# Performance work log

Measured on AMD Instinct MI355X. Metric: run time of the kernel, lower is better.

Reference implementation:

```python
import jax, jax.numpy as jnp
import numpy as np

HIDDEN = 128
NUM_VAL = 100000
NUM_CST = 20000
NUM_EDGES = 500000
LN_EPS = 1e-5


def layer_norm(x, g, b):
    mu = jnp.mean(x, axis=-1, keepdims=True)
    var = jnp.var(x, axis=-1, keepdims=True)
    return (x - mu) * jax.lax.rsqrt(var + LN_EPS) * g + b


def setup_inputs() -> dict:
    key = jax.random.key(0)
    ks = jax.random.split(key, 8)
    h_val = jax.random.normal(ks[0], (NUM_VAL, HIDDEN), dtype=jnp.float32)
    assign = jax.random.uniform(ks[1], (NUM_VAL,), dtype=jnp.float32)
    cst_src = jax.random.randint(ks[2], (NUM_EDGES,), 0, NUM_CST)  # constraint idx (scatter target)
    cst_dst = jax.random.randint(ks[3], (NUM_EDGES,), 0, NUM_VAL)  # value idx (gather source)
    LE = jax.random.randint(ks[4], (NUM_EDGES,), 0, 2)
    PE = jax.random.randint(ks[5], (NUM_EDGES,), 0, 2)
    s1 = 1.0 / np.sqrt(HIDDEN + 1)
    s2 = 1.0 / np.sqrt(HIDDEN)
    W1 = jax.random.normal(ks[6], (HIDDEN + 1, HIDDEN), dtype=jnp.float32) * s1
    b1 = jnp.zeros((HIDDEN,), dtype=jnp.float32)
    k7, k8 = jax.random.split(ks[7])
    W2 = jax.random.normal(k7, (HIDDEN, HIDDEN), dtype=jnp.float32) * s2
    W3 = jax.random.normal(k8, (HIDDEN, 4 * HIDDEN), dtype=jnp.float32) * s2
    return {
        "h_val": h_val, "assign": assign,
        "cst_src": cst_src, "cst_dst": cst_dst, "LE": LE, "PE": PE,
        "W1": W1, "b1": b1, "W2": W2,
        "ln1_g": jnp.ones((HIDDEN,), jnp.float32), "ln1_b": jnp.zeros((HIDDEN,), jnp.float32),
        "W3": W3,
        "ln2_g": jnp.ones((4 * HIDDEN,), jnp.float32), "ln2_b": jnp.zeros((4 * HIDDEN,), jnp.float32),
    }


def reference(h_val, assign, cst_src, cst_dst, LE, PE, W1, b1, W2, ln1_g, ln1_b, W3, ln2_g, ln2_b):
    # val_enc: Linear -> ReLU -> Linear(no bias) -> LayerNorm
    x = jnp.concatenate([h_val, assign[:, None]], axis=1)  # [V, H+1]
    x_val = layer_norm(jax.nn.relu(x @ W1 + b1) @ W2, ln1_g, ln1_b)  # [V, H]
    # val_send: Linear(no bias) -> LayerNorm over 4H, then view as [4V, H]
    m_val = layer_norm(x_val @ W3, ln2_g, ln2_b).reshape(4 * NUM_VAL, HIDDEN)
    # gather by composite edge index, scatter-sum into constraints
    out_idx = 4 * cst_dst + 2 * LE + PE  # [E]
    msg = m_val[out_idx]  # [E, H]
    r_cst = jax.ops.segment_sum(msg, cst_src, num_segments=NUM_CST)  # [C, H]
    return (r_cst, x_val)
```

## Files before the change

### kernel.cpp

```cpp
#include <hip/hip_runtime.h>
#include <hip/hip_bf16.h>

#define HID 128
#define NVAL 100000
#define NCST 20000
#define NEDGE 500000
#define LN_EPS 1e-5f
#define BCAP 96

#define ENC_BLOCKS  ((NVAL + 63) / 64)
#define SEND_BLOCKS (NVAL / 32)
#define WPACK_BLOCKS 48
#define SCT_BLOCKS  ((NEDGE + 255) / 256)

typedef __attribute__((ext_vector_type(8))) short bf16x8;
typedef __attribute__((ext_vector_type(4))) float f32x4;

static __device__ __forceinline__ unsigned short f2bf(float x) {
    union { float f; unsigned int u; } a; a.f = x;
    const unsigned int r = a.u + 0x7FFF + ((a.u >> 16) & 1);
    return (unsigned short)(r >> 16);
}
static __device__ __forceinline__ float bf2f(unsigned short u) {
    union { unsigned int i; float f; } x; x.i = (unsigned int)u << 16; return x.f;
}

__global__ __launch_bounds__(256) void k_phase1(
    const float* __restrict__ W1, const float* __restrict__ W2,
    const float* __restrict__ W3,
    unsigned short* __restrict__ PW1, unsigned short* __restrict__ PW2,
    unsigned short* __restrict__ PW3,
    const int* __restrict__ cst_src, const int* __restrict__ cst_dst,
    const int* __restrict__ LE, const int* __restrict__ PE,
    int* __restrict__ cnt, int* __restrict__ rows2)
{
    if (blockIdx.x < WPACK_BLOCKS) {
        const int g = blockIdx.x * 256 + threadIdx.x;
        const float* W; unsigned short* P; int gg, ncol;
        if (g < 2048)      { W = W1; P = PW1; gg = g;        ncol = 128; }
        else if (g < 4096) { W = W2; P = PW2; gg = g - 2048; ncol = 128; }
        else               { W = W3; P = PW3; gg = g - 4096; ncol = 512; }
        const int ct = gg >> 8, kc = (gg >> 6) & 3, l = gg & 63;
        const int col = ct * 16 + (l & 15);
        const int k0  = kc * 32 + (l >> 4) * 8;
        unsigned short tmp[8];
        #pragma unroll
        for (int j = 0; j < 8; ++j)
            tmp[j] = f2bf(W[(size_t)(k0 + j) * ncol + col]);
        *(bf16x8*)&P[(size_t)gg * 8] = *(const bf16x8*)tmp;
    } else {
        const int i = (blockIdx.x - WPACK_BLOCKS) * 256 + threadIdx.x;
        if (i < NEDGE) {
            const int s = cst_src[i];
            const int p = atomicAdd(&cnt[s], 1);
            if (p < BCAP)
                rows2[s * BCAP + p] = 4 * cst_dst[i] + 2 * LE[i] + PE[i];
        }
    }
}

__global__ __launch_bounds__(256) void k_val_enc_mfma(
    const float* __restrict__ h_val, const float* __restrict__ assign,
    const unsigned short* __restrict__ PW1, const float* __restrict__ W1,
    const float* __restrict__ b1, const unsigned short* __restrict__ PW2,
    const float* __restrict__ g1, const float* __restrict__ bb1,
    float* __restrict__ x_val, unsigned short* __restrict__ xb, int use_xb)
{
    __shared__ __align__(16) unsigned short AsHs[2 * 64 * 136];
    __shared__ float red[4][64][2];
    __shared__ float assn[64];

    unsigned short* As = AsHs;
    unsigned short* Hs = AsHs + 64 * 136;
    float* Os = (float*)AsHs;

    const int tid  = threadIdx.x;
    const int w    = tid >> 6;
    const int l    = tid & 63;
    const int row0 = blockIdx.x * 64;

    {
        const int r  = tid >> 2;
        const int c0 = (tid & 3) * 32;
        if (row0 + r < NVAL) {
            const float* src = h_val + (size_t)(row0 + r) * HID + c0;
            #pragma unroll
            for (int i = 0; i < 4; ++i) {
                const float4 va = *(const float4*)(src + i * 8);
                const float4 vb = *(const float4*)(src + i * 8 + 4);
                unsigned short h[8] = { f2bf(va.x), f2bf(va.y), f2bf(va.z), f2bf(va.w),
                                        f2bf(vb.x), f2bf(vb.y), f2bf(vb.z), f2bf(vb.w) };
                *(bf16x8*)&As[r * 136 + c0 + i * 8] = *(const bf16x8*)h;
            }
        } else {
            unsigned short z[8] = {0,0,0,0,0,0,0,0};
            #pragma unroll
            for (int i = 0; i < 4; ++i)
                *(bf16x8*)&As[r * 136 + c0 + i * 8] = *(const bf16x8*)z;
        }
    }
    if (tid < 64) assn[tid] = (row0 + tid < NVAL) ? assign[row0 + tid] : 0.0f;

    float b1c[2], wrc[2], g1c[2], bbc[2];
    #pragma unroll
    for (int ct = 0; ct < 2; ++ct) {
        const int col = (w * 2 + ct) * 16 + (l & 15);
        b1c[ct] = b1[col];
        wrc[ct] = W1[(size_t)128 * HID + col];
        g1c[ct] = g1[col];
        bbc[ct] = bb1[col];
    }

    __syncthreads();

    const int arow = l & 15;
    const int akb  = (l >> 4) * 8;

    f32x4 acc[4][2];
    #pragma unroll
    for (int rt = 0; rt < 4; ++rt)
        #pragma unroll
        for (int ct = 0; ct < 2; ++ct) acc[rt][ct] = (f32x4){0.f, 0.f, 0.f, 0.f};
    #pragma unroll
    for (int kc = 0; kc < 4; ++kc) {
        bf16x8 a[4];
        #pragma unroll
        for (int rt = 0; rt < 4; ++rt)
            a[rt] = *(const bf16x8*)&As[(arow + rt * 16) * 136 + kc * 32 + akb];
        #pragma unroll
        for (int ct = 0; ct < 2; ++ct) {
            const int ctg = w * 2 + ct;
            const bf16x8 b = *(const bf16x8*)&PW1[(size_t)((ctg * 4 + kc) * 64 + l) * 8];
            #pragma unroll
            for (int rt = 0; rt < 4; ++rt)
                acc[rt][ct] = __builtin_amdgcn_mfma_f32_16x16x32_bf16(a[rt], b, acc[rt][ct], 0, 0, 0);
        }
    }

    #pragma unroll
    for (int rt = 0; rt < 4; ++rt)
        #pragma unroll
        for (int ct = 0; ct < 2; ++ct) {
            const int col = (w * 2 + ct) * 16 + (l & 15);
            #pragma unroll
            for (int q = 0; q < 4; ++q) {
                const int row = rt * 16 + (l >> 4) * 4 + q;
                float v = acc[rt][ct][q] + b1c[ct] + assn[row] * wrc[ct];
                v = fmaxf(v, 0.0f);
                Hs[row * 136 + col] = f2bf(v);
            }
        }
    __syncthreads();

    f32x4 acc2[4][2];
    #pragma unroll
    for (int rt = 0; rt < 4; ++rt)
        #pragma unroll
        for (int ct = 0; ct < 2; ++ct) acc2[rt][ct] = (f32x4){0.f, 0.f, 0.f, 0.f};
    #pragma unroll
    for (int kc = 0; kc < 4; ++kc) {
        bf16x8 a[4];
        #pragma unroll
        for (int rt = 0; rt < 4; ++rt)
            a[rt] = *(const bf16x8*)&Hs[(arow + rt * 16) * 136 + kc * 32 + akb];
        #pragma unroll
        for (int ct = 0; ct < 2; ++ct) {
            const int ctg = w * 2 + ct;
            const bf16x8 b = *(const bf16x8*)&PW2[(size_t)((ctg * 4 + kc) * 64 + l) * 8];
            #pragma unroll
            for (int rt = 0; rt < 4; ++rt)
                acc2[rt][ct] = __builtin_amdgcn_mfma_f32_16x16x32_bf16(a[rt], b, acc2[rt][ct], 0, 0, 0);
        }
    }

    #pragma unroll
    for (int rt = 0; rt < 4; ++rt)
        #pragma unroll
        for (int q = 0; q < 4; ++q) {
            float s  = acc2[rt][0][q] + acc2[rt][1][q];
            float qq = acc2[rt][0][q] * acc2[rt][0][q] + acc2[rt][1][q] * acc2[rt][1][q];
            #pragma unroll
            for (int off2 = 1; off2 < 16; off2 <<= 1) {
                s  += __shfl_xor(s,  off2);
                qq += __shfl_xor(qq, off2);
            }
            if ((l & 15) == 0) {
                const int row = rt * 16 + (l >> 4) * 4 + q;
                red[w][row][0] = s;
                red[w][row][1] = qq;
            }
        }
    __syncthreads();

    #pragma unroll
    for (int rt = 0; rt < 4; ++rt)
        #pragma unroll
        for (int q = 0; q < 4; ++q) {
            const int row = rt * 16 + (l >> 4) * 4 + q;
            const float S = red[0][row][0] + red[1][row][0] + red[2][row][0] + red[3][row][0];
            const float Q = red[0][row][1] + red[1][row][1] + red[2][row][1] + red[3][row][1];
            const float mu  = S * (1.0f / 128.0f);
            const float var = Q * (1.0f / 128.0f) - mu * mu;
            const float rs  = rsqrtf(var + LN_EPS);
            #pragma unroll
            for (int ct = 0; ct < 2; ++ct) {
                const int col = (w * 2 + ct) * 16 + (l & 15);
                Os[row * 132 + col] = (acc2[rt][ct][q] - mu) * rs * g1c[ct] + bbc[ct];
            }
        }
    __syncthreads();

    {
        const int r  = tid >> 2;
        const int c0 = (tid & 3) * 32;
        if (row0 + r < NVAL) {
            float* dst = x_val + (size_t)(row0 + r) * HID + c0;
            #pragma unroll
            for (int i = 0; i < 8; ++i)
                *(float4*)(dst + i * 4) = *(const float4*)&Os[r * 132 + c0 + i * 4];
            if (use_xb) {
                unsigned short* db = xb + (size_t)(row0 + r) * HID + c0;
                #pragma unroll
                for (int i = 0; i < 4; ++i) {
                    const float4 va = *(const float4*)&Os[r * 132 + c0 + i * 8];
                    const float4 vb = *(const float4*)&Os[r * 132 + c0 + i * 8 + 4];
                    unsigned short h[8] = { f2bf(va.x), f2bf(va.y), f2bf(va.z), f2bf(va.w),
                                            f2bf(vb.x), f2bf(vb.y), f2bf(vb.z), f2bf(vb.w) };
                    *(bf16x8*)&db[i * 8] = *(const bf16x8*)h;
                }
            }
        }
    }
}

__global__ __launch_bounds__(256) void k_send(
    const float* __restrict__ x_val, const unsigned short* __restrict__ xb,
    const unsigned short* __restrict__ PB,
    const float* __restrict__ g2, const float* __restrict__ b2,
    unsigned short* __restrict__ m_val, int use_xb)
{
    __shared__ __align__(16) unsigned short U[16 * 520];
    __shared__ float red[4][32][2];

    unsigned short* As   = U;
    unsigned short* Os2h = U;

    const int tid  = threadIdx.x;
    const int w    = tid >> 6;
    const int l    = tid & 63;
    const int row0 = blockIdx.x * 32;

    if (use_xb) {
        const int r  = tid >> 3;
        const int c0 = (tid & 7) * 16;
        const unsigned short* src = xb + (size_t)(row0 + r) * HID + c0;
        *(bf16x8*)&As[r * 136 + c0]     = *(const bf16x8*)&src[0];
        *(bf16x8*)&As[r * 136 + c0 + 8] = *(const bf16x8*)&src[8];
    } else {
        const int r  = tid >> 3;
        const int c0 = (tid & 7) * 16;
        const float* src = x_val + (size_t)(row0 + r) * HID + c0;
        #pragma unroll
        for (int i = 0; i < 4; ++i) {
            const float4 v = *(const float4*)(src + i * 4);
            unsigned short h[4] = { f2bf(v.x), f2bf(v.y), f2bf(v.z), f2bf(v.w) };
            *(ushort4*)&As[r * 136 + c0 + i * 4] = *(const ushort4*)h;
        }
    }

    float ga[8], bb[8];
    #pragma unroll
    for (int ct = 0; ct < 8; ++ct) {
        const int col = (w * 8 + ct) * 16 + (l & 15);
        ga[ct] = g2[col];
        bb[ct] = b2[col];
    }

    f32x4 acc[2][8];
    #pragma unroll
    for (int rt = 0; rt < 2; ++rt)
        #pragma unroll
        for (int ct = 0; ct < 8; ++ct)
            acc[rt][ct] = (f32x4){0.f, 0.f, 0.f, 0.f};

    __syncthreads();

    const int arow = l & 15;
    const int akb  = (l >> 4) * 8;
    #pragma unroll
    for (int kc = 0; kc < 4; ++kc) {
        const bf16x8 a0 = *(const bf16x8*)&As[(arow +  0) * 136 + kc * 32 + akb];
        const bf16x8 a1 = *(const bf16x8*)&As[(arow + 16) * 136 + kc * 32 + akb];
        #pragma unroll
        for (int ct = 0; ct < 8; ++ct) {
            const int ctg = w * 8 + ct;
            const bf16x8 b = *(const bf16x8*)&PB[(size_t)((ctg * 4 + kc) * 64 + l) * 8];
            acc[0][ct] = __builtin_amdgcn_mfma_f32_16x16x32_bf16(a0, b, acc[0][ct], 0, 0, 0);
            acc[1][ct] = __builtin_amdgcn_mfma_f32_16x16x32_bf16(a1, b, acc[1][ct], 0, 0, 0);
        }
    }

    float ps[2][4], pq[2][4];
    #pragma unroll
    for (int rt = 0; rt < 2; ++rt)
        #pragma unroll
        for (int q = 0; q < 4; ++q) {
            float s = 0.f, qq = 0.f;
            #pragma unroll
            for (int ct = 0; ct < 8; ++ct) {
                const float v = acc[rt][ct][q];
                s += v; qq += v * v;
            }
            #pragma unroll
            for (int off2 = 1; off2 < 16; off2 <<= 1) {
                s  += __shfl_xor(s,  off2);
                qq += __shfl_xor(qq, off2);
            }
            ps[rt][q] = s; pq[rt][q] = qq;
        }
    if ((l & 15) == 0) {
        #pragma unroll
        for (int rt = 0; rt < 2; ++rt)
            #pragma unroll
            for (int q = 0; q < 4; ++q) {
                const int row = rt * 16 + (l >> 4) * 4 + q;
                red[w][row][0] = ps[rt][q];
                red[w][row][1] = pq[rt][q];
            }
    }
    __syncthreads();

    #pragma unroll
    for (int rt = 0; rt < 2; ++rt) {
        #pragma unroll
        for (int q = 0; q < 4; ++q) {
            const int rl  = (l >> 4) * 4 + q;
            const int row = rt * 16 + rl;
            const float S = red[0][row][0] + red[1][row][0] + red[2][row][0] + red[3][row][0];
            const float Q = red[0][row][1] + red[1][row][1] + red[2][row][1] + red[3][row][1];
            const float mu  = S * (1.0f / 512.0f);
            const float var = Q * (1.0f / 512.0f) - mu * mu;
            const float rs  = rsqrtf(var + LN_EPS);
            #pragma unroll
            for (int ct = 0; ct < 8; ++ct) {
                const int col = (w * 8 + ct) * 16 + (l & 15);
                const float v = (acc[rt][ct][q] - mu) * rs * ga[ct] + bb[ct];
                Os2h[rl * 520 + col] = f2bf(v);
            }
        }
        __syncthreads();
        #pragma unroll
        for (int i = 0; i < 4; ++i) {
            const int flat = i * 2048 + tid * 8;
            const int r = flat >> 9, c = flat & 511;
            *(bf16x8*)&m_val[(size_t)(row0 + rt * 16 + r) * 512 + c] =
                *(const bf16x8*)&Os2h[r * 520 + c];
        }
        __syncthreads();
    }
}

__global__ __launch_bounds__(64) void k_accum(
    const int* __restrict__ cnt, const int* __restrict__ rows2,
    const unsigned short* __restrict__ m_val, float* __restrict__ r_cst)
{
    const int c = blockIdx.x;
    const int l = threadIdx.x;
    const int n = min(cnt[c], BCAP);
    const int start = c * BCAP;
    const int slot = l >> 4;
    const int c8   = (l & 15) * 8;

    float a0=0.f,a1=0.f,a2=0.f,a3=0.f,a4=0.f,a5=0.f,a6=0.f,a7=0.f;
    for (int j = slot; j < n; j += 4) {
        const int row = rows2[start + j];
        const uint4 v = *(const uint4*)&m_val[(size_t)row * HID + c8];
        a0 += bf2f((unsigned short)(v.x & 0xFFFF));
        a1 += bf2f((unsigned short)(v.x >> 16));
        a2 += bf2f((unsigned short)(v.y & 0xFFFF));
        a3 += bf2f((unsigned short)(v.y >> 16));
        a4 += bf2f((unsigned short)(v.z & 0xFFFF));
        a5 += bf2f((unsigned short)(v.z >> 16));
        a6 += bf2f((unsigned short)(v.w & 0xFFFF));
        a7 += bf2f((unsigned short)(v.w >> 16));
    }
    a0 += __shfl_xor(a0, 16); a0 += __shfl_xor(a0, 32);
    a1 += __shfl_xor(a1, 16); a1 += __shfl_xor(a1, 32);
    a2 += __shfl_xor(a2, 16); a2 += __shfl_xor(a2, 32);
    a3 += __shfl_xor(a3, 16); a3 += __shfl_xor(a3, 32);
    a4 += __shfl_xor(a4, 16); a4 += __shfl_xor(a4, 32);
    a5 += __shfl_xor(a5, 16); a5 += __shfl_xor(a5, 32);
    a6 += __shfl_xor(a6, 16); a6 += __shfl_xor(a6, 32);
    a7 += __shfl_xor(a7, 16); a7 += __shfl_xor(a7, 32);
    if (l < 16) {
        const float4 o0 = {a0, a1, a2, a3};
        const float4 o1 = {a4, a5, a6, a7};
        *(float4*)&r_cst[(size_t)c * HID + c8]     = o0;
        *(float4*)&r_cst[(size_t)c * HID + c8 + 4] = o1;
    }
}

__global__ __launch_bounds__(128) void k_val_enc(
    const float* __restrict__ h_val, const float* __restrict__ assign,
    const float* __restrict__ W1, const float* __restrict__ b1,
    const float* __restrict__ W2,
    const float* __restrict__ g1, const float* __restrict__ bb1,
    float* __restrict__ x_val)
{
    const int R = 32;
    __shared__ __align__(16) float xs[R * 132];
    __shared__ float red[R][2][2];

    const int tid  = threadIdx.x;
    const int row0 = blockIdx.x * R;

    #pragma unroll 4
    for (int r = 0; r < R; ++r)
        xs[r * 132 + tid] = h_val[(size_t)(row0 + r) * HID + tid];
    if (tid < R) xs[tid * 132 + 128] = assign[row0 + tid];
    __syncthreads();

    float acc[R];
    {
        const float bias = b1[tid];
        #pragma unroll
        for (int r = 0; r < R; ++r) acc[r] = bias;
    }
    for (int k = 0; k < 128; k += 4) {
        const float w0 = W1[(k + 0) * HID + tid];
        const float w1 = W1[(k + 1) * HID + tid];
        const float w2 = W1[(k + 2) * HID + tid];
        const float w3 = W1[(k + 3) * HID + tid];
        #pragma unroll
        for (int r = 0; r < R; ++r) {
            const float4 x4 = *(const float4*)&xs[r * 132 + k];
            acc[r] = fmaf(x4.x, w0, acc[r]);
            acc[r] = fmaf(x4.y, w1, acc[r]);
            acc[r] = fmaf(x4.z, w2, acc[r]);
            acc[r] = fmaf(x4.w, w3, acc[r]);
        }
    }
    {
        const float w = W1[128 * HID + tid];
        #pragma unroll
        for (int r = 0; r < R; ++r) acc[r] = fmaf(xs[r * 132 + 128], w, acc[r]);
    }
    #pragma unroll
    for (int r = 0; r < R; ++r) acc[r] = fmaxf(acc[r], 0.0f);

    __syncthreads();
    #pragma unroll
    for (int r = 0; r < R; ++r) xs[r * 132 + tid] = acc[r];
    __syncthreads();

    float acc2[R];
    #pragma unroll
    for (int r = 0; r < R; ++r) acc2[r] = 0.0f;
    for (int k = 0; k < 128; k += 4) {
        const float w0 = W2[(k + 0) * HID + tid];
        const float w1 = W2[(k + 1) * HID + tid];
        const float w2 = W2[(k + 2) * HID + tid];
        const float w3 = W2[(k + 3) * HID + tid];
        #pragma unroll
        for (int r = 0; r < R; ++r) {
            const float4 x4 = *(const float4*)&xs[r * 132 + k];
            acc2[r] = fmaf(x4.x, w0, acc2[r]);
            acc2[r] = fmaf(x4.y, w1, acc2[r]);
            acc2[r] = fmaf(x4.z, w2, acc2[r]);
            acc2[r] = fmaf(x4.w, w3, acc2[r]);
        }
    }

    const int lane = tid & 63, wid = tid >> 6;
    #pragma unroll
    for (int r = 0; r < R; ++r) {
        float s = acc2[r];
        float q = acc2[r] * acc2[r];
        #pragma unroll
        for (int off = 32; off > 0; off >>= 1) {
            s += __shfl_xor(s, off);
            q += __shfl_xor(q, off);
        }
        if (lane == 0) { red[r][wid][0] = s; red[r][wid][1] = q; }
    }
    __syncthreads();
    const float g = g1[tid], bb = bb1[tid];
    #pragma unroll
    for (int r = 0; r < R; ++r) {
        const float s  = red[r][0][0] + red[r][1][0];
        const float q  = red[r][0][1] + red[r][1][1];
        const float mu = s * (1.0f / 128.0f);
        const float var = q * (1.0f / 128.0f) - mu * mu;
        const float rs = rsqrtf(var + LN_EPS);
        x_val[(size_t)(row0 + r) * HID + tid] = (acc2[r] - mu) * rs * g + bb;
    }
}

__global__ __launch_bounds__(256) void k_val_send(
    const float* __restrict__ x_val, const float* __restrict__ W3,
    const float* __restrict__ g2, const float* __restrict__ b2,
    __hip_bfloat16* __restrict__ m_val)
{
    const int R = 32;
    __shared__ __align__(16) float xs[R * 132];
    __shared__ float red[R][4][2];

    const int tid  = threadIdx.x;
    const int row0 = blockIdx.x * R;

    for (int i = tid; i < R * HID; i += 256) {
        const int r = i >> 7, c = i & 127;
        xs[r * 132 + c] = x_val[(size_t)(row0 + r) * HID + c];
    }
    __syncthreads();

    float a0[R], a1[R];
    #pragma unroll
    for (int r = 0; r < R; ++r) { a0[r] = 0.0f; a1[r] = 0.0f; }

    for (int k = 0; k < 128; k += 2) {
        const float w00 = W3[(size_t)(k + 0) * 512 + tid];
        const float w01 = W3[(size_t)(k + 0) * 512 + tid + 256];
        const float w10 = W3[(size_t)(k + 1) * 512 + tid];
        const float w11 = W3[(size_t)(k + 1) * 512 + tid + 256];
        #pragma unroll
        for (int r = 0; r < R; ++r) {
            const float2 x2 = *(const float2*)&xs[r * 132 + k];
            a0[r] = fmaf(x2.x, w00, a0[r]);
            a1[r] = fmaf(x2.x, w01, a1[r]);
            a0[r] = fmaf(x2.y, w10, a0[r]);
            a1[r] = fmaf(x2.y, w11, a1[r]);
        }
    }

    const int lane = tid & 63, wid = tid >> 6;
    #pragma unroll
    for (int r = 0; r < R; ++r) {
        float s = a0[r] + a1[r];
        float q = a0[r] * a0[r] + a1[r] * a1[r];
        #pragma unroll
        for (int off = 32; off > 0; off >>= 1) {
            s += __shfl_xor(s, off);
            q += __shfl_xor(q, off);
        }
        if (lane == 0) { red[r][wid][0] = s; red[r][wid][1] = q; }
    }
    __syncthreads();
    const float ga = g2[tid], gb = g2[tid + 256];
    const float ba = b2[tid], bbv = b2[tid + 256];
    #pragma unroll
    for (int r = 0; r < R; ++r) {
        const float s  = red[r][0][0] + red[r][1][0] + red[r][2][0] + red[r][3][0];
        const float q  = red[r][0][1] + red[r][1][1] + red[r][2][1] + red[r][3][1];
        const float mu = s * (1.0f / 512.0f);
        const float var = q * (1.0f / 512.0f) - mu * mu;
        const float rs = rsqrtf(var + LN_EPS);
        const size_t base = (size_t)(row0 + r) * 512;
        m_val[base + tid]       = __float2bfloat16((a0[r] - mu) * rs * ga + ba);
        m_val[base + tid + 256] = __float2bfloat16((a1[r] - mu) * rs * gb + bbv);
    }
}

__global__ __launch_bounds__(256) void k_edge(
    const int* __restrict__ cst_src, const int* __restrict__ cst_dst,
    const int* __restrict__ LE, const int* __restrict__ PE,
    const __hip_bfloat16* __restrict__ m_val,
    float* __restrict__ r_cst)
{
    const int wave = (blockIdx.x * 256 + threadIdx.x) >> 6;
    const int lane = threadIdx.x & 63;
    if (wave >= NEDGE) return;

    const int s   = cst_src[wave];
    const int row = 4 * cst_dst[wave] + 2 * LE[wave] + PE[wave];

    const __hip_bfloat16* mp = m_val + (size_t)row * HID + lane * 2;
    const float v0 = __bfloat162float(mp[0]);
    const float v1 = __bfloat162float(mp[1]);

    float* out = r_cst + (size_t)s * HID + lane * 2;
    atomicAdd(out + 0, v0);
    atomicAdd(out + 1, v1);
}

extern "C" void kernel_launch(void* const* d_in, const int* in_sizes, int n_in,
                              void* d_out, int out_size, void* d_ws, size_t ws_size,
                              hipStream_t stream) {
    const float* h_val   = (const float*)d_in[0];
    const float* assign  = (const float*)d_in[1];
    const int*   cst_src = (const int*)d_in[2];
    const int*   cst_dst = (const int*)d_in[3];
    const int*   LE      = (const int*)d_in[4];
    const int*   PE      = (const int*)d_in[5];
    const float* W1      = (const float*)d_in[6];
    const float* b1      = (const float*)d_in[7];
    const float* W2      = (const float*)d_in[8];
    const float* g1      = (const float*)d_in[9];
    const float* bb1     = (const float*)d_in[10];
    const float* W3      = (const float*)d_in[11];
    const float* g2      = (const float*)d_in[12];
    const float* b2      = (const float*)d_in[13];

    float* r_cst = (float*)d_out;
    float* x_val = (float*)d_out + (size_t)NCST * HID;

    char* ws = (char*)d_ws;
    const size_t MVAL_B   = (size_t)4 * NVAL * HID * sizeof(__hip_bfloat16);
    const size_t CNT_OFF  = MVAL_B;
    const size_t RW2_OFF  = (CNT_OFF + (size_t)NCST * 4 + 255) & ~(size_t)255;
    const size_t PW3_OFF  = (RW2_OFF + (size_t)NCST * BCAP * 4 + 255) & ~(size_t)255;
    const size_t PW1_OFF  = PW3_OFF + (size_t)128 * 512 * 2;
    const size_t PW2_OFF  = PW1_OFF + (size_t)128 * 128 * 2;
    const size_t NEED_ALL = PW2_OFF + (size_t)128 * 128 * 2;
    const size_t XB_OFF   = (NEED_ALL + 255) & ~(size_t)255;
    const size_t NEED_XB  = XB_OFF + (size_t)NVAL * HID * 2;

    __hip_bfloat16* m_val = (__hip_bfloat16*)ws;
    int* cnt    = (int*)(ws + CNT_OFF);
    int* rows2  = (int*)(ws + RW2_OFF);
    unsigned short* PW3 = (unsigned short*)(ws + PW3_OFF);
    unsigned short* PW1 = (unsigned short*)(ws + PW1_OFF);
    unsigned short* PW2 = (unsigned short*)(ws + PW2_OFF);
    unsigned short* xb  = (unsigned short*)(ws + XB_OFF);

    const bool full_ok = (ws_size >= NEED_ALL);
    const int  use_xb  = (ws_size >= NEED_XB) ? 1 : 0;

    if (full_ok) {
        hipMemsetAsync(cnt, 0, (size_t)NCST * 4, stream);
        k_phase1<<<WPACK_BLOCKS + SCT_BLOCKS, 256, 0, stream>>>(
            W1, W2, W3, PW1, PW2, PW3, cst_src, cst_dst, LE, PE, cnt, rows2);
        k_val_enc_mfma<<<ENC_BLOCKS, 256, 0, stream>>>(
            h_val, assign, PW1, W1, b1, PW2, g1, bb1, x_val, xb, use_xb);
        k_send<<<SEND_BLOCKS, 256, 0, stream>>>(
            x_val, xb, PW3, g2, b2, (unsigned short*)m_val, use_xb);
        k_accum<<<NCST, 64, 0, stream>>>(cnt, rows2, (const unsigned short*)m_val, r_cst);
    } else {
        k_val_enc<<<NVAL / 32, 128, 0, stream>>>(h_val, assign, W1, b1, W2, g1, bb1, x_val);
        k_val_send<<<NVAL / 32, 256, 0, stream>>>(x_val, W3, g2, b2, (__hip_bfloat16*)m_val);
        hipMemsetAsync(d_out, 0, (size_t)NCST * HID * sizeof(float), stream);
        k_edge<<<NEDGE / 4, 256, 0, stream>>>(cst_src, cst_dst, LE, PE, (const __hip_bfloat16*)m_val, r_cst);
    }
}
```

Baseline: 157.9 us.

## Split encoder and send kernels into halves to overlap enc and send stages

The encoder and send stages are split at a row boundary into three launches: the first half of the encoder, a mixed kernel that runs the second half of the encoder alongside the first half of send, and the second half of send. Encoder and send are independent per row, so this fills GPU tail and idle time by co-scheduling memory-bound and compute-bound blocks within one launch. The mixed kernel always reserves the larger encoder shared-memory footprint for every block, which can lower occupancy for the send blocks, and it adds one extra launch.

```diff
diff --git a/kernel.cpp b/kernel.cpp
--- a/kernel.cpp
+++ b/kernel.cpp
@@ -13,6 +13,15 @@
 #define WPACK_BLOCKS 48
 #define SCT_BLOCKS  ((NEDGE + 255) / 256)
 
+#define SPLIT_ROWS   49984
+#define ENC_A_BLOCKS 781
+#define ENC_B_BLOCKS (ENC_BLOCKS - ENC_A_BLOCKS)
+#define SEND_A_BLOCKS 1562
+#define SEND_B_BLOCKS (SEND_BLOCKS - SEND_A_BLOCKS)
+
+#define ENC_SMEM  37120
+#define SEND_SMEM 17664
+
 typedef __attribute__((ext_vector_type(8))) short bf16x8;
 typedef __attribute__((ext_vector_type(4))) float f32x4;
 
@@ -25,59 +34,23 @@
     union { unsigned int i; float f; } x; x.i = (unsigned int)u << 16; return x.f;
 }
 
-__global__ __launch_bounds__(256) void k_phase1(
-    const float* __restrict__ W1, const float* __restrict__ W2,
-    const float* __restrict__ W3,
-    unsigned short* __restrict__ PW1, unsigned short* __restrict__ PW2,
-    unsigned short* __restrict__ PW3,
-    const int* __restrict__ cst_src, const int* __restrict__ cst_dst,
-    const int* __restrict__ LE, const int* __restrict__ PE,
-    int* __restrict__ cnt, int* __restrict__ rows2)
-{
-    if (blockIdx.x < WPACK_BLOCKS) {
-        const int g = blockIdx.x * 256 + threadIdx.x;
-        const float* W; unsigned short* P; int gg, ncol;
-        if (g < 2048)      { W = W1; P = PW1; gg = g;        ncol = 128; }
-        else if (g < 4096) { W = W2; P = PW2; gg = g - 2048; ncol = 128; }
-        else               { W = W3; P = PW3; gg = g - 4096; ncol = 512; }
-        const int ct = gg >> 8, kc = (gg >> 6) & 3, l = gg & 63;
-        const int col = ct * 16 + (l & 15);
-        const int k0  = kc * 32 + (l >> 4) * 8;
-        unsigned short tmp[8];
-        #pragma unroll
-        for (int j = 0; j < 8; ++j)
-            tmp[j] = f2bf(W[(size_t)(k0 + j) * ncol + col]);
-        *(bf16x8*)&P[(size_t)gg * 8] = *(const bf16x8*)tmp;
-    } else {
-        const int i = (blockIdx.x - WPACK_BLOCKS) * 256 + threadIdx.x;
-        if (i < NEDGE) {
-            const int s = cst_src[i];
-            const int p = atomicAdd(&cnt[s], 1);
-            if (p < BCAP)
-                rows2[s * BCAP + p] = 4 * cst_dst[i] + 2 * LE[i] + PE[i];
-        }
-    }
-}
-
-__global__ __launch_bounds__(256) void k_val_enc_mfma(
+static __device__ __forceinline__ void enc_body(
+    char* smem, int row0, int tid,
     const float* __restrict__ h_val, const float* __restrict__ assign,
     const unsigned short* __restrict__ PW1, const float* __restrict__ W1,
     const float* __restrict__ b1, const unsigned short* __restrict__ PW2,
     const float* __restrict__ g1, const float* __restrict__ bb1,
     float* __restrict__ x_val, unsigned short* __restrict__ xb, int use_xb)
 {
-    __shared__ __align__(16) unsigned short AsHs[2 * 64 * 136];
-    __shared__ float red[4][64][2];
-    __shared__ float assn[64];
-
-    unsigned short* As = AsHs;
-    unsigned short* Hs = AsHs + 64 * 136;
-    float* Os = (float*)AsHs;
-
-    const int tid  = threadIdx.x;
-    const int w    = tid >> 6;
-    const int l    = tid & 63;
-    const int row0 = blockIdx.x * 64;
+    unsigned short* As = (unsigned short*)smem;
+    unsigned short* Hs = As + 64 * 136;
+    float* Os = (float*)smem;
+    typedef float red_t[64][2];
+    red_t* red = (red_t*)(smem + 34816);
+    float* assn = (float*)(smem + 34816 + 2048);
+
+    const int w = tid >> 6;
+    const int l = tid & 63;
 
     {
         const int r  = tid >> 2;
@@ -233,22 +206,20 @@
     }
 }
 
-__global__ __launch_bounds__(256) void k_send(
+static __device__ __forceinline__ void send_body(
+    char* smem, int row0, int tid,
     const float* __restrict__ x_val, const unsigned short* __restrict__ xb,
     const unsigned short* __restrict__ PB,
     const float* __restrict__ g2, const float* __restrict__ b2,
     unsigned short* __restrict__ m_val, int use_xb)
 {
-    __shared__ __align__(16) unsigned short U[16 * 520];
-    __shared__ float red[4][32][2];
-
-    unsigned short* As   = U;
-    unsigned short* Os2h = U;
-
-    const int tid  = threadIdx.x;
-    const int w    = tid >> 6;
-    const int l    = tid & 63;
-    const int row0 = blockIdx.x * 32;
+    unsigned short* As   = (unsigned short*)smem;
+    unsigned short* Os2h = (unsigned short*)smem;
+    typedef float red_t[32][2];
+    red_t* red = (red_t*)(smem + 16640);
+
+    const int w = tid >> 6;
+    const int l = tid & 63;
 
     if (use_xb) {
         const int r  = tid >> 3;
@@ -358,6 +329,84 @@
         }
         __syncthreads();
     }
+}
+
+__global__ __launch_bounds__(256) void k_phase1(
+    const float* __restrict__ W1, const float* __restrict__ W2,
+    const float* __restrict__ W3,
+    unsigned short* __restrict__ PW1, unsigned short* __restrict__ PW2,
+    unsigned short* __restrict__ PW3,
+    const int* __restrict__ cst_src, const int* __restrict__ cst_dst,
+    const int* __restrict__ LE, const int* __restrict__ PE,
+    int* __restrict__ cnt, int* __restrict__ rows2)
+{
+    if (blockIdx.x < WPACK_BLOCKS) {
+        const int g = blockIdx.x * 256 + threadIdx.x;
+        const float* W; unsigned short* P; int gg, ncol;
+        if (g < 2048)      { W = W1; P = PW1; gg = g;        ncol = 128; }
+        else if (g < 4096) { W = W2; P = PW2; gg = g - 2048; ncol = 128; }
+        else               { W = W3; P = PW3; gg = g - 4096; ncol = 512; }
+        const int ct = gg >> 8, kc = (gg >> 6) & 3, l = gg & 63;
+        const int col = ct * 16 + (l & 15);
+        const int k0  = kc * 32 + (l >> 4) * 8;
+        unsigned short tmp[8];
+        #pragma unroll
+        for (int j = 0; j < 8; ++j)
+            tmp[j] = f2bf(W[(size_t)(k0 + j) * ncol + col]);
+        *(bf16x8*)&P[(size_t)gg * 8] = *(const bf16x8*)tmp;
+    } else {
+        const int i = (blockIdx.x - WPACK_BLOCKS) * 256 + threadIdx.x;
+        if (i < NEDGE) {
+            const int s = cst_src[i];
+            const int p = atomicAdd(&cnt[s], 1);
+            if (p < BCAP)
+                rows2[s * BCAP + p] = 4 * cst_dst[i] + 2 * LE[i] + PE[i];
+        }
+    }
+}
+
+__global__ __launch_bounds__(256) void k_enc_part(
+    const float* __restrict__ h_val, const float* __restrict__ assign,
+    const unsigned short* __restrict__ PW1, const float* __restrict__ W1,
+    const float* __restrict__ b1, const unsigned short* __restrict__ PW2,
+    const float* __restrict__ g1, const float* __restrict__ bb1,
+    float* __restrict__ x_val, unsigned short* __restrict__ xb, int use_xb,
+    int row_base)
+{
+    __shared__ __align__(16) char smem[ENC_SMEM];
+    enc_body(smem, row_base + blockIdx.x * 64, threadIdx.x,
+             h_val, assign, PW1, W1, b1, PW2, g1, bb1, x_val, xb, use_xb);
+}
+
+__global__ __launch_bounds__(256) void k_mid(
+    const float* __restrict__ h_val, const float* __restrict__ assign,
+    const unsigned short* __restrict__ PW1, const float* __restrict__ W1,
+    const float* __restrict__ b1, const unsigned short* __restrict__ PW2,
+    const float* __restrict__ g1, const float* __restrict__ bb1,
+    float* __restrict__ x_val, unsigned short* __restrict__ xb, int use_xb,
+    const unsigned short* __restrict__ PW3,
+    const float* __restrict__ g2, const float* __restrict__ b2,
+    unsigned short* __restrict__ m_val)
+{
+    __shared__ __align__(16) char smem[ENC_SMEM];
+    if (blockIdx.x < ENC_B_BLOCKS) {
+        enc_body(smem, SPLIT_ROWS + blockIdx.x * 64, threadIdx.x,
+                 h_val, assign, PW1, W1, b1, PW2, g1, bb1, x_val, xb, use_xb);
+    } else {
+        send_body(smem, (blockIdx.x - ENC_B_BLOCKS) * 32, threadIdx.x,
+                  x_val, xb, PW3, g2, b2, m_val, use_xb);
+    }
+}
+
+__global__ __launch_bounds__(256) void k_send_part(
+    const float* __restrict__ x_val, const unsigned short* __restrict__ xb,
+    const unsigned short* __restrict__ PB,
+    const float* __restrict__ g2, const float* __restrict__ b2,
+    unsigned short* __restrict__ m_val, int use_xb, int row_base)
+{
+    __shared__ __align__(16) char smem[SEND_SMEM];
+    send_body(smem, row_base + blockIdx.x * 32, threadIdx.x,
+              x_val, xb, PB, g2, b2, m_val, use_xb);
 }
 
 __global__ __launch_bounds__(64) void k_accum(
@@ -630,10 +679,13 @@
         hipMemsetAsync(cnt, 0, (size_t)NCST * 4, stream);
         k_phase1<<<WPACK_BLOCKS + SCT_BLOCKS, 256, 0, stream>>>(
             W1, W2, W3, PW1, PW2, PW3, cst_src, cst_dst, LE, PE, cnt, rows2);
-        k_val_enc_mfma<<<ENC_BLOCKS, 256, 0, stream>>>(
-            h_val, assign, PW1, W1, b1, PW2, g1, bb1, x_val, xb, use_xb);
-        k_send<<<SEND_BLOCKS, 256, 0, stream>>>(
-            x_val, xb, PW3, g2, b2, (unsigned short*)m_val, use_xb);
+        k_enc_part<<<ENC_A_BLOCKS, 256, 0, stream>>>(
+            h_val, assign, PW1, W1, b1, PW2, g1, bb1, x_val, xb, use_xb, 0);
+        k_mid<<<ENC_B_BLOCKS + SEND_A_BLOCKS, 256, 0, stream>>>(
+            h_val, assign, PW1, W1, b1, PW2, g1, bb1, x_val, xb, use_xb,
+            PW3, g2, b2, (unsigned short*)m_val);
+        k_send_part<<<SEND_B_BLOCKS, 256, 0, stream>>>(
+            x_val, xb, PW3, g2, b2, (unsigned short*)m_val, use_xb, SPLIT_ROWS);
         k_accum<<<NCST, 64, 0, stream>>>(cnt, rows2, (const unsigned short*)m_val, r_cst);
     } else {
         k_val_enc<<<NVAL / 32, 128, 0, stream>>>(h_val, assign, W1, b1, W2, g1, bb1, x_val);
```

Measured after the change: 177.5 us. +12.4%, slower.
